# Performance work log

Measured on AMD Instinct MI355X. Metric: run time of the kernel, lower is better.

## Reference

```python
import jax, jax.numpy as jnp
import numpy as np

C = 192
B, H, W = 16, 64, 64
FILTERS = (1, 3, 3, 3, 1)
INIT_SCALE = 10.0
LIKELIHOOD_BOUND = 1e-6


def setup_inputs() -> dict:
    key = jax.random.key(0)
    kx, *kb = jax.random.split(key, 6)
    x = jax.random.normal(kx, (B, C, H, W), dtype=jnp.float32)
    scale = INIT_SCALE ** (1.0 / (len(FILTERS) - 1))
    inp = {"x": x}
    for i in range(4):
        init = float(np.log(np.expm1(1.0 / scale / FILTERS[i + 1])))
        inp[f"m{i}"] = jnp.full((C, FILTERS[i + 1], FILTERS[i]), init, dtype=jnp.float32)
        inp[f"b{i}"] = jax.random.uniform(kb[i], (C, FILTERS[i + 1], 1), minval=-0.5, maxval=0.5, dtype=jnp.float32)
    for i in range(3):
        inp[f"f{i}"] = jnp.zeros((C, FILTERS[i + 1], 1), dtype=jnp.float32)
    return inp


def _logits_cumulative(logits, mats, biases, factors):
    # logits: (C, 1, N); mats[i]: (C, f_out, f_in)
    for i in range(len(mats)):
        m = jax.nn.softplus(mats[i])
        logits = jnp.einsum('coi,cin->con', m, logits) + biases[i]
        if i < len(factors):
            logits = logits + jnp.tanh(factors[i]) * jnp.tanh(logits)
    return logits


def reference(x, m0, m1, m2, m3, b0, b1, b2, b3, f0, f1, f2):
    mats = (m0, m1, m2, m3)
    biases = (b0, b1, b2, b3)
    factors = (f0, f1, f2)
    b, c, h, w = x.shape
    xt = jnp.transpose(x, (1, 0, 2, 3)).reshape(c, 1, -1)  # (C,1,N)
    lower = _logits_cumulative(xt - 0.5, mats, biases, factors)
    upper = _logits_cumulative(xt + 0.5, mats, biases, factors)
    sign = jax.lax.stop_gradient(-jnp.sign(lower + upper))
    likelihood = jnp.abs(jax.nn.sigmoid(sign * upper) - jax.nn.sigmoid(sign * lower))
    likelihood = jnp.maximum(likelihood, LIKELIHOOD_BOUND)  # Low_bound forward = clamp
    likelihood = likelihood.reshape(c, b, h, w)
    return jnp.transpose(likelihood, (1, 0, 2, 3))
```

## Files before the change

kernel.cpp:

```cpp
#include <hip/hip_runtime.h>
#include <cmath>

#define NCH 192
#define SLAB 4096
#define LUT_N 2048
#define LUT_XMIN (-8.0f)
#define LUT_H (16.0f / (float)LUT_N)
#define LUT_INVH ((float)LUT_N / 16.0f)
#define LUT_OFF (-(LUT_XMIN) * LUT_INVH)

__device__ __forceinline__ float sigmoidf_(float x) {
    return 1.0f / (1.0f + __expf(-x));
}

__device__ __forceinline__ float softplusf_(float x) {
    return (x > 20.0f) ? x : log1pf(expf(x));
}

__device__ __forceinline__ float mlp_eval(const float* __restrict__ p, float z,
                                          bool g0, bool g1, bool g2) {
    float t0 = fmaf(p[0], z, p[24]);
    float t1 = fmaf(p[1], z, p[25]);
    float t2 = fmaf(p[2], z, p[26]);
    if (g0) {
        t0 += p[34] * tanhf(t0);
        t1 += p[35] * tanhf(t1);
        t2 += p[36] * tanhf(t2);
    }
    float u0 = fmaf(p[3], t0, fmaf(p[4], t1, fmaf(p[5], t2, p[27])));
    float u1 = fmaf(p[6], t0, fmaf(p[7], t1, fmaf(p[8], t2, p[28])));
    float u2 = fmaf(p[9], t0, fmaf(p[10], t1, fmaf(p[11], t2, p[29])));
    if (g1) {
        u0 += p[37] * tanhf(u0);
        u1 += p[38] * tanhf(u1);
        u2 += p[39] * tanhf(u2);
    }
    float w0 = fmaf(p[12], u0, fmaf(p[13], u1, fmaf(p[14], u2, p[30])));
    float w1 = fmaf(p[15], u0, fmaf(p[16], u1, fmaf(p[17], u2, p[31])));
    float w2 = fmaf(p[18], u0, fmaf(p[19], u1, fmaf(p[20], u2, p[32])));
    if (g2) {
        w0 += p[40] * tanhf(w0);
        w1 += p[41] * tanhf(w1);
        w2 += p[42] * tanhf(w2);
    }
    return fmaf(p[21], w0, fmaf(p[22], w1, fmaf(p[23], w2, p[33])));
}

__device__ __forceinline__ float element(const float* __restrict__ p, float v,
                                         bool g0, bool g1, bool g2) {
    float lo = mlp_eval(p, v - 0.5f, g0, g1, g2);
    float up = mlp_eval(p, v + 0.5f, g0, g1, g2);
    float ssum = lo + up;
    float s = (ssum > 0.0f) ? -1.0f : ((ssum < 0.0f) ? 1.0f : 0.0f);
    float lk = fabsf(sigmoidf_(s * up) - sigmoidf_(s * lo));
    return fmaxf(lk, 1e-6f);
}

__device__ __forceinline__ void stage_params(
    float* p, int c, int tid,
    const float* __restrict__ m0, const float* __restrict__ b0,
    const float* __restrict__ m1, const float* __restrict__ b1,
    const float* __restrict__ m2, const float* __restrict__ b2,
    const float* __restrict__ m3, const float* __restrict__ b3,
    const float* __restrict__ f0, const float* __restrict__ f1,
    const float* __restrict__ f2)
{
    if (tid < 43) {
        float v;
        if (tid < 3)       v = softplusf_(m0[c * 3 + tid]);
        else if (tid < 12) v = softplusf_(m1[c * 9 + (tid - 3)]);
        else if (tid < 21) v = softplusf_(m2[c * 9 + (tid - 12)]);
        else if (tid < 24) v = softplusf_(m3[c * 3 + (tid - 21)]);
        else if (tid < 27) v = b0[c * 3 + (tid - 24)];
        else if (tid < 30) v = b1[c * 3 + (tid - 27)];
        else if (tid < 33) v = b2[c * 3 + (tid - 30)];
        else if (tid < 34) v = b3[c];
        else if (tid < 37) v = tanhf(f0[c * 3 + (tid - 34)]);
        else if (tid < 40) v = tanhf(f1[c * 3 + (tid - 37)]);
        else               v = tanhf(f2[c * 3 + (tid - 40)]);
        p[tid] = v;
    }
}

__global__ __launch_bounds__(256) void build_lut_kernel(
    const float* __restrict__ m0, const float* __restrict__ b0,
    const float* __restrict__ m1, const float* __restrict__ b1,
    const float* __restrict__ m2, const float* __restrict__ b2,
    const float* __restrict__ m3, const float* __restrict__ b3,
    const float* __restrict__ f0, const float* __restrict__ f1,
    const float* __restrict__ f2,
    float2* __restrict__ lut)
{
    __shared__ float p[43];
    __shared__ float vals[LUT_N + 1];
    const int c   = blockIdx.x;
    const int tid = threadIdx.x;

    stage_params(p, c, tid, m0, b0, m1, b1, m2, b2, m3, b3, f0, f1, f2);
    __syncthreads();

    const bool g0 = (p[34] != 0.0f) | (p[35] != 0.0f) | (p[36] != 0.0f);
    const bool g1 = (p[37] != 0.0f) | (p[38] != 0.0f) | (p[39] != 0.0f);
    const bool g2 = (p[40] != 0.0f) | (p[41] != 0.0f) | (p[42] != 0.0f);

    for (int i = tid; i <= LUT_N; i += 256) {
        float xv = fmaf((float)i, LUT_H, LUT_XMIN);
        vals[i] = element(p, xv, g0, g1, g2);
    }
    __syncthreads();

    float2* dst = lut + (size_t)c * LUT_N;
    for (int i = tid; i < LUT_N; i += 256) {
        float2 e;
        e.x = vals[i];
        e.y = vals[i + 1] - vals[i];
        dst[i] = e;
    }
}

__global__ __launch_bounds__(256) void eb_lut_kernel(
    const float* __restrict__ x,
    const float2* __restrict__ lut,
    float* __restrict__ out)
{
    __shared__ float2 l[LUT_N];
    const int bc  = blockIdx.x;
    const int c   = bc % NCH;
    const int tid = threadIdx.x;

    const float4* __restrict__ src4 = (const float4*)(lut + (size_t)c * LUT_N);
    float4* l4 = (float4*)l;
#pragma unroll
    for (int i = 0; i < 4; ++i) l4[tid + i * 256] = src4[tid + i * 256];
    __syncthreads();

    const size_t base = (size_t)bc * SLAB;
    const float4* __restrict__ xin = (const float4*)(x + base);
    float4* __restrict__ o = (float4*)(out + base);

#pragma unroll
    for (int i = 0; i < 4; ++i) {
        const int idx = tid + i * 256;
        float4 v = xin[idx];
        float4 r;
        {
            float t = fmaf(v.x, LUT_INVH, LUT_OFF);
            t = fminf(fmaxf(t, 0.0f), (float)(LUT_N - 1));
            float tf = floorf(t);
            float2 e = l[(int)tf];
            r.x = fmaf(t - tf, e.y, e.x);
        }
        {
            float t = fmaf(v.y, LUT_INVH, LUT_OFF);
            t = fminf(fmaxf(t, 0.0f), (float)(LUT_N - 1));
            float tf = floorf(t);
            float2 e = l[(int)tf];
            r.y = fmaf(t - tf, e.y, e.x);
        }
        {
            float t = fmaf(v.z, LUT_INVH, LUT_OFF);
            t = fminf(fmaxf(t, 0.0f), (float)(LUT_N - 1));
            float tf = floorf(t);
            float2 e = l[(int)tf];
            r.z = fmaf(t - tf, e.y, e.x);
        }
        {
            float t = fmaf(v.w, LUT_INVH, LUT_OFF);
            t = fminf(fmaxf(t, 0.0f), (float)(LUT_N - 1));
            float tf = floorf(t);
            float2 e = l[(int)tf];
            r.w = fmaf(t - tf, e.y, e.x);
        }
        o[idx] = r;
    }
}

__global__ __launch_bounds__(256) void eb_kernel(
    const float* __restrict__ x,
    const float* __restrict__ m0, const float* __restrict__ b0,
    const float* __restrict__ m1, const float* __restrict__ b1,
    const float* __restrict__ m2, const float* __restrict__ b2,
    const float* __restrict__ m3, const float* __restrict__ b3,
    const float* __restrict__ f0, const float* __restrict__ f1,
    const float* __restrict__ f2,
    float* __restrict__ out)
{
    __shared__ float p[43];
    const int bc  = blockIdx.x;
    const int c   = bc % NCH;
    const int tid = threadIdx.x;

    stage_params(p, c, tid, m0, b0, m1, b1, m2, b2, m3, b3, f0, f1, f2);
    __syncthreads();

    const bool g0 = (p[34] != 0.0f) | (p[35] != 0.0f) | (p[36] != 0.0f);
    const bool g1 = (p[37] != 0.0f) | (p[38] != 0.0f) | (p[39] != 0.0f);
    const bool g2 = (p[40] != 0.0f) | (p[41] != 0.0f) | (p[42] != 0.0f);

    const size_t base = (size_t)bc * SLAB;
    const float4* __restrict__ xin = (const float4*)(x + base);
    float4* __restrict__ o = (float4*)(out + base);

#pragma unroll
    for (int i = 0; i < 4; ++i) {
        const int idx = tid + i * 256;
        float4 v = xin[idx];
        float4 r;
        r.x = element(p, v.x, g0, g1, g2);
        r.y = element(p, v.y, g0, g1, g2);
        r.z = element(p, v.z, g0, g1, g2);
        r.w = element(p, v.w, g0, g1, g2);
        o[idx] = r;
    }
}

extern "C" void kernel_launch(void* const* d_in, const int* in_sizes, int n_in,
                              void* d_out, int out_size, void* d_ws, size_t ws_size,
                              hipStream_t stream) {
    const float* x = (const float*)d_in[0];
    const float *m0, *m1, *m2, *m3, *b0, *b1, *b2, *b3;
    if (in_sizes[2] == 1728) {
        m0 = (const float*)d_in[1]; m1 = (const float*)d_in[2];
        m2 = (const float*)d_in[3]; m3 = (const float*)d_in[4];
        b0 = (const float*)d_in[5]; b1 = (const float*)d_in[6];
        b2 = (const float*)d_in[7]; b3 = (const float*)d_in[8];
    } else {
        m0 = (const float*)d_in[1]; b0 = (const float*)d_in[2];
        m1 = (const float*)d_in[3]; b1 = (const float*)d_in[4];
        m2 = (const float*)d_in[5]; b2 = (const float*)d_in[6];
        m3 = (const float*)d_in[7]; b3 = (const float*)d_in[8];
    }
    const float* f0 = (const float*)d_in[9];
    const float* f1 = (const float*)d_in[10];
    const float* f2 = (const float*)d_in[11];
    float* out = (float*)d_out;

    const int nblocks = out_size / SLAB;
    const size_t lut_bytes = (size_t)NCH * LUT_N * sizeof(float2);

    if (ws_size >= lut_bytes) {
        float2* lut = (float2*)d_ws;
        build_lut_kernel<<<NCH, 256, 0, stream>>>(m0, b0, m1, b1, m2, b2, m3, b3,
                                                  f0, f1, f2, lut);
        eb_lut_kernel<<<nblocks, 256, 0, stream>>>(x, lut, out);
    } else {
        eb_kernel<<<nblocks, 256, 0, stream>>>(x, m0, b0, m1, b1, m2, b2, m3, b3,
                                               f0, f1, f2, out);
    }
}
```

Before: 128.9 us.

## Halve LUT size, parallelize LUT build across blocks, use nontemporal stores

Halves the per-channel lookup table to 1024 entries and splits the LUT build across four blocks per channel, each thread computing one entry and its neighbor directly instead of staging through shared memory. The aim is to shorten the serial build kernel and the per-block LUT load into LDS. The main kernel now writes output with nontemporal stores to reduce cache pollution. The coarser table increases interpolation error, and each entry's neighbor value is now computed twice.

```diff
diff --git a/kernel.cpp b/kernel.cpp
--- a/kernel.cpp
+++ b/kernel.cpp
@@ -3,11 +3,13 @@
 
 #define NCH 192
 #define SLAB 4096
-#define LUT_N 2048
+#define LUT_N 1024
 #define LUT_XMIN (-8.0f)
 #define LUT_H (16.0f / (float)LUT_N)
 #define LUT_INVH ((float)LUT_N / 16.0f)
 #define LUT_OFF (-(LUT_XMIN) * LUT_INVH)
+
+typedef float f4_t __attribute__((ext_vector_type(4)));
 
 __device__ __forceinline__ float sigmoidf_(float x) {
     return 1.0f / (1.0f + __expf(-x));
@@ -92,9 +94,10 @@
     float2* __restrict__ lut)
 {
     __shared__ float p[43];
-    __shared__ float vals[LUT_N + 1];
-    const int c   = blockIdx.x;
-    const int tid = threadIdx.x;
+    const int c    = blockIdx.x >> 2;
+    const int seg  = blockIdx.x & 3;
+    const int tid  = threadIdx.x;
+    const int i    = seg * 256 + tid;
 
     stage_params(p, c, tid, m0, b0, m1, b1, m2, b2, m3, b3, f0, f1, f2);
     __syncthreads();
@@ -103,19 +106,14 @@
     const bool g1 = (p[37] != 0.0f) | (p[38] != 0.0f) | (p[39] != 0.0f);
     const bool g2 = (p[40] != 0.0f) | (p[41] != 0.0f) | (p[42] != 0.0f);
 
-    for (int i = tid; i <= LUT_N; i += 256) {
-        float xv = fmaf((float)i, LUT_H, LUT_XMIN);
-        vals[i] = element(p, xv, g0, g1, g2);
-    }
-    __syncthreads();
-
-    float2* dst = lut + (size_t)c * LUT_N;
-    for (int i = tid; i < LUT_N; i += 256) {
-        float2 e;
-        e.x = vals[i];
-        e.y = vals[i + 1] - vals[i];
-        dst[i] = e;
-    }
+    const float x0 = fmaf((float)i, LUT_H, LUT_XMIN);
+    const float v0 = element(p, x0, g0, g1, g2);
+    const float v1 = element(p, x0 + LUT_H, g0, g1, g2);
+
+    float2 e;
+    e.x = v0;
+    e.y = v1 - v0;
+    lut[(size_t)c * LUT_N + i] = e;
 }
 
 __global__ __launch_bounds__(256) void eb_lut_kernel(
@@ -130,19 +128,19 @@
 
     const float4* __restrict__ src4 = (const float4*)(lut + (size_t)c * LUT_N);
     float4* l4 = (float4*)l;
-#pragma unroll
-    for (int i = 0; i < 4; ++i) l4[tid + i * 256] = src4[tid + i * 256];
+    l4[tid] = src4[tid];
+    l4[tid + 256] = src4[tid + 256];
     __syncthreads();
 
     const size_t base = (size_t)bc * SLAB;
     const float4* __restrict__ xin = (const float4*)(x + base);
-    float4* __restrict__ o = (float4*)(out + base);
+    f4_t* __restrict__ o = (f4_t*)(out + base);
 
 #pragma unroll
     for (int i = 0; i < 4; ++i) {
         const int idx = tid + i * 256;
         float4 v = xin[idx];
-        float4 r;
+        f4_t r;
         {
             float t = fmaf(v.x, LUT_INVH, LUT_OFF);
             t = fminf(fmaxf(t, 0.0f), (float)(LUT_N - 1));
@@ -171,7 +169,7 @@
             float2 e = l[(int)tf];
             r.w = fmaf(t - tf, e.y, e.x);
         }
-        o[idx] = r;
+        __builtin_nontemporal_store(r, &o[idx]);
     }
 }
 
@@ -240,8 +238,8 @@
 
     if (ws_size >= lut_bytes) {
         float2* lut = (float2*)d_ws;
-        build_lut_kernel<<<NCH, 256, 0, stream>>>(m0, b0, m1, b1, m2, b2, m3, b3,
-                                                  f0, f1, f2, lut);
+        build_lut_kernel<<<NCH * (LUT_N / 256), 256, 0, stream>>>(
+            m0, b0, m1, b1, m2, b2, m3, b3, f0, f1, f2, lut);
         eb_lut_kernel<<<nblocks, 256, 0, stream>>>(x, lut, out);
     } else {
         eb_kernel<<<nblocks, 256, 0, stream>>>(x, m0, b0, m1, b1, m2, b2, m3, b3,
```

After: 128.7 us. No clear change (-0.1%).
